# Kernel tuning notes

Hardware: AMD Instinct MI355X
Metric: run time of the kernel (lower is better)

## Reference

```python
import jax, jax.numpy as jnp
import numpy as np

B, D, T, K = 32, 64, 4096, 512
COMMITMENT_COST = 0.25


def setup_inputs() -> dict:
    key = jax.random.key(0)
    k1, k2 = jax.random.split(key)
    z = jax.random.normal(k1, (B, D, T), dtype=jnp.float32)
    # nn.Embedding init: uniform(-1/K, 1/K)
    codebook = jax.random.uniform(k2, (K, D), dtype=jnp.float32,
                                  minval=-1.0 / K, maxval=1.0 / K)
    return {"z": z, "codebook": codebook}


def reference(z, codebook):
    sg = jax.lax.stop_gradient
    zt = jnp.transpose(z, (0, 2, 1))            # [B, T, D]
    zf = zt.reshape(-1, D)                      # [N, D], N = B*T
    # squared L2 distances: ||z||^2 + ||e||^2 - 2 z.e  -> [N, K]
    dists = (jnp.sum(zf * zf, axis=1, keepdims=True)
             + jnp.sum(codebook * codebook, axis=1)
             - 2.0 * jnp.matmul(zf, codebook.T))
    idx = jnp.argmin(dists, axis=1)             # [N]
    # gather codebook rows (same math as one-hot @ codebook)
    quantized = codebook[idx].reshape(zt.shape)  # [B, T, D]
    codebook_loss = jnp.mean((sg(quantized) - zt) ** 2)
    commitment_loss = jnp.mean((quantized - sg(zt)) ** 2)
    vq_loss = codebook_loss + COMMITMENT_COST * commitment_loss
    # straight-through estimator
    quantized_st = zt + sg(quantized - zt)
    quantized_out = jnp.transpose(quantized_st, (0, 2, 1))  # [B, D, T]
    indices = idx.reshape(B, T)
    return vq_loss, quantized_out, indices
```

## Files before the change

### kernel.cpp

```cpp
#include <hip/hip_runtime.h>

#define NB 32
#define ND 64
#define NT 4096
#define NK 512
#define NGRID 1024

typedef __attribute__((ext_vector_type(8))) short short8;
typedef __attribute__((ext_vector_type(16))) float f32x16;
typedef unsigned int uint32;
typedef unsigned short ushort16_t;

#define PERM(r) ((((r) & 7) * 16) + ((r) >> 3))
#define STR 68
#define ESTR 66
#define M2 2.5e-4f
#define RCAP 4
#define NSLOT 16

__device__ __forceinline__ ushort16_t bf16rne(float f) {
    uint32 u = __float_as_uint(f);
    return (ushort16_t)((u + 0x7FFFu + ((u >> 16) & 1u)) >> 16);
}
__device__ __forceinline__ float bf16tof(ushort16_t h) {
    return __uint_as_float(((uint32)h) << 16);
}

__global__ void prep_kernel(const float* __restrict__ cb,
                            uint4* __restrict__ cbfrag,
                            float* __restrict__ enorm,
                            double* __restrict__ loss_acc,
                            uint32* __restrict__ counter) {
    const int bi = blockIdx.x, tid = threadIdx.x;
    if (bi < 16) {
        const int t = bi * 256 + tid;
        const int c = t >> 8, rem = t & 255, s = rem >> 6, L = rem & 63;
        const int kcode = c * 32 + (L & 31);
        const int dbase = s * 16 + ((L >> 5) << 3);
        const float* src = cb + (size_t)kcode * 64 + dbase;
        const float4 pa = *(const float4*)src;
        const float4 pb = *(const float4*)(src + 4);
        const float f[8] = {pa.x, pa.y, pa.z, pa.w, pb.x, pb.y, pb.z, pb.w};
        uint32 hw[4], lw[4];
#pragma unroll
        for (int i = 0; i < 4; ++i) {
            const ushort16_t h0 = bf16rne(f[2*i]);
            const ushort16_t h1 = bf16rne(f[2*i+1]);
            const ushort16_t l0 = bf16rne(f[2*i]   - bf16tof(h0));
            const ushort16_t l1 = bf16rne(f[2*i+1] - bf16tof(h1));
            hw[i] = (uint32)h0 | ((uint32)h1 << 16);
            lw[i] = (uint32)l0 | ((uint32)l1 << 16);
        }
        cbfrag[(size_t)((c*4+s)*2 + 0)*64 + L] = make_uint4(hw[0],hw[1],hw[2],hw[3]);
        cbfrag[(size_t)((c*4+s)*2 + 1)*64 + L] = make_uint4(lw[0],lw[1],lw[2],lw[3]);
    } else {
        if (tid < NSLOT) loss_acc[tid] = 0.0;
        if (tid == 0) *counter = 0u;
        for (int k = tid; k < NK; k += 256) {
            const float* e = cb + (size_t)k * ND;
            float r[8];
#pragma unroll
            for (int j = 0; j < 8; ++j) {
                float s = __fmul_rn(e[j], e[j]);
#pragma unroll
                for (int i = 1; i < 8; ++i)
                    s = __fadd_rn(s, __fmul_rn(e[8*i+j], e[8*i+j]));
                r[j] = s;
            }
            enorm[k] = __fadd_rn(__fadd_rn(__fadd_rn(r[0],r[1]), __fadd_rn(r[2],r[3])),
                                 __fadd_rn(__fadd_rn(r[4],r[5]), __fadd_rn(r[6],r[7])));
        }
    }
}

__device__ __forceinline__ float exact_dist(const float* __restrict__ zrow,
                                            const float* __restrict__ cb,
                                            const float* __restrict__ enl,
                                            float zn, int k2) {
    const float4* e4 = (const float4*)(cb + (size_t)k2 * ND);
    float a = 0.0f;
#pragma unroll
    for (int w = 0; w < 16; ++w) {
        const float4 ev = e4[w];
        const float4 zv = *(const float4*)(zrow + 4 * w);
        a = __builtin_fmaf(zv.x, ev.x, a);
        a = __builtin_fmaf(zv.y, ev.y, a);
        a = __builtin_fmaf(zv.z, ev.z, a);
        a = __builtin_fmaf(zv.w, ev.w, a);
    }
    return __fsub_rn(__fadd_rn(zn, enl[k2]), __fmul_rn(2.0f, a));
}

__global__ __launch_bounds__(256, 3) void vq_main(const float* __restrict__ z,
                                                  const float* __restrict__ cb,
                                                  const uint4* __restrict__ cbfrag,
                                                  const float* __restrict__ enorm,
                                                  float* __restrict__ qout,
                                                  float* __restrict__ idxout,
                                                  double* __restrict__ loss_acc,
                                                  uint32* __restrict__ counter,
                                                  float* __restrict__ out0) {
    __shared__ __align__(16) char smem[39968];
    float*       zl   = (float*)smem;
    float*       enl  = (float*)(smem + 34816);
    float*       znl  = (float*)(smem + 36864);
    ushort16_t*  cand = (ushort16_t*)(smem + 37376);
    int*         sfin = (int*)(smem + 39424);
    double*      sred = (double*)(smem + 39936);

    const int bi    = blockIdx.x;
    const int b     = bi >> 5;
    const int tbase = (bi & 31) * 128;
    const int tid   = threadIdx.x;
    const size_t zoff = (size_t)b * (ND * NT) + tbase;

#pragma unroll
    for (int j = 0; j < 8; ++j) {
        const int qq = j * 256 + tid;
        const int i4 = qq & 31, d = qq >> 5;
        const float4 v = *(const float4*)(z + zoff + (size_t)d * NT + i4 * 4);
        const float vv[4] = {v.x, v.y, v.z, v.w};
#pragma unroll
        for (int c = 0; c < 4; ++c) {
            const int r = i4 * 4 + c;
            zl[PERM(r) * STR + d] = vv[c];
        }
    }
    for (int k = tid; k < NK; k += 256) enl[k] = enorm[k];
    __syncthreads();

    if (tid < 128) {
        const int r = tid;
        const float4* zr4 = (const float4*)&zl[PERM(r) * STR];
        float x[64];
#pragma unroll
        for (int wq = 0; wq < 16; ++wq) {
            const float4 t4 = zr4[wq];
            x[4*wq] = t4.x; x[4*wq+1] = t4.y; x[4*wq+2] = t4.z; x[4*wq+3] = t4.w;
        }
        float r8[8];
#pragma unroll
        for (int jj = 0; jj < 8; ++jj) {
            float s = __fmul_rn(x[jj], x[jj]);
#pragma unroll
            for (int ii = 1; ii < 8; ++ii)
                s = __fadd_rn(s, __fmul_rn(x[8*ii+jj], x[8*ii+jj]));
            r8[jj] = s;
        }
        znl[r] = __fadd_rn(__fadd_rn(__fadd_rn(r8[0],r8[1]), __fadd_rn(r8[2],r8[3])),
                           __fadd_rn(__fadd_rn(r8[4],r8[5]), __fadd_rn(r8[6],r8[7])));
    }

    const int L    = tid & 63;
    const int w    = tid >> 6;
    const int h    = L >> 5;
    const int rowl = w * 32 + (L & 31);
    short8 bhf[4], blf[4];
    {
        const float* zrow = &zl[PERM(rowl) * STR];
#pragma unroll
        for (int s = 0; s < 4; ++s) {
            const int d0 = s * 16 + h * 8;
            const float4 pa = *(const float4*)(zrow + d0);
            const float4 pb = *(const float4*)(zrow + d0 + 4);
            const float f[8] = {pa.x, pa.y, pa.z, pa.w, pb.x, pb.y, pb.z, pb.w};
            uint32 hw[4], lw[4];
#pragma unroll
            for (int i = 0; i < 4; ++i) {
                const ushort16_t h0 = bf16rne(f[2*i]);
                const ushort16_t h1 = bf16rne(f[2*i+1]);
                const ushort16_t l0 = bf16rne(f[2*i]   - bf16tof(h0));
                const ushort16_t l1 = bf16rne(f[2*i+1] - bf16tof(h1));
                hw[i] = (uint32)h0 | ((uint32)h1 << 16);
                lw[i] = (uint32)l0 | ((uint32)l1 << 16);
            }
            union { uint4 u; short8 s8; } uh, ul;
            uh.u = make_uint4(hw[0],hw[1],hw[2],hw[3]);
            ul.u = make_uint4(lw[0],lw[1],lw[2],lw[3]);
            bhf[s] = uh.s8; blf[s] = ul.s8;
        }
    }
    __syncthreads();

    const int h4 = h * 4;

    uint32 p1 = 0u, p2 = 0u, p3 = 0u;
#pragma unroll 2
    for (int c = 0; c < 16; ++c) {
        uint4 B[8];
#pragma unroll
        for (int p = 0; p < 8; ++p) B[p] = cbfrag[(size_t)((c * 8 + p) * 64) + L];
        f32x16 acc0, acc1;
#pragma unroll
        for (int r = 0; r < 16; ++r) { acc0[r] = 0.0f; acc1[r] = 0.0f; }
#pragma unroll
        for (int s = 0; s < 4; ++s) {
            union { uint4 u; short8 s8; } ah, al;
            ah.u = B[s * 2 + 0];
            al.u = B[s * 2 + 1];
            acc0 = __builtin_amdgcn_mfma_f32_32x32x16_bf16(ah.s8, bhf[s], acc0, 0, 0, 0);
            acc0 = __builtin_amdgcn_mfma_f32_32x32x16_bf16(al.s8, bhf[s], acc0, 0, 0, 0);
            acc1 = __builtin_amdgcn_mfma_f32_32x32x16_bf16(ah.s8, blf[s], acc1, 0, 0, 0);
        }
#pragma unroll
        for (int r = 0; r < 16; ++r) {
            const int kc = c * 32 + ((r & 3) + 8 * (r >> 2)) + h4;
            const float a = acc0[r] + acc1[r];
            const uint32 pv = (__float_as_uint(fmaxf(a + 1.0f, 0.0f)) & ~0x1FFu)
                            | (uint32)kc;
            const bool g1 = pv > p1, g2 = pv > p2, g3 = pv > p3;
            p3 = g2 ? p2 : (g3 ? pv : p3);
            p2 = g1 ? p1 : (g2 ? pv : p2);
            p1 = g1 ? pv : p1;
        }
    }

    const uint32 op1 = __shfl_xor(p1, 32);
    const uint32 pkG = (p1 > op1) ? p1 : op1;
    const int    kG  = (int)(pkG & 0x1FFu);
    const float  bm   = __uint_as_float(pkG & ~0x1FFu) - 1.0f;
    const float  thrf = bm - M2;
    const uint32 thrF = __float_as_uint(fmaxf(thrf + 1.0f, 0.0f)) & ~0x1FFu;

    const float* zrow = &zl[PERM(rowl) * STR];
    const float  zn   = znl[rowl];
    const int    iown = (((kG >> 2) & 1) == h);

    int bkf;
    if (__any((int)(p3 >= thrF))) {
        int myc = 0, ovf = 0;
        ushort16_t* mylist = cand + (rowl * 2 + h) * RCAP;
#pragma unroll 1
        for (int c = 0; c < 16; ++c) {
            uint4 B[8];
#pragma unroll
            for (int p = 0; p < 8; ++p) B[p] = cbfrag[(size_t)((c * 8 + p) * 64) + L];
            f32x16 acc0, acc1;
#pragma unroll
            for (int r = 0; r < 16; ++r) { acc0[r] = 0.0f; acc1[r] = 0.0f; }
#pragma unroll
            for (int s = 0; s < 4; ++s) {
                union { uint4 u; short8 s8; } ah, al;
                ah.u = B[s * 2 + 0];
                al.u = B[s * 2 + 1];
                acc0 = __builtin_amdgcn_mfma_f32_32x32x16_bf16(ah.s8, bhf[s], acc0, 0, 0, 0);
                acc0 = __builtin_amdgcn_mfma_f32_32x32x16_bf16(al.s8, bhf[s], acc0, 0, 0, 0);
                acc1 = __builtin_amdgcn_mfma_f32_32x32x16_bf16(ah.s8, blf[s], acc1, 0, 0, 0);
            }
#pragma unroll
            for (int r = 0; r < 16; ++r) {
                const int kc = c * 32 + ((r & 3) + 8 * (r >> 2)) + h4;
                const float a = acc0[r] + acc1[r];
                const uint32 pv = (__float_as_uint(fmaxf(a + 1.0f, 0.0f)) & ~0x1FFu)
                                | (uint32)kc;
                if (pv >= thrF && kc != kG) {
                    if (myc < RCAP) mylist[myc++] = (ushort16_t)kc;
                    else ovf = 1;
                }
            }
        }
        const int totr = myc + __shfl_xor(myc, 32);
        const int aovf = ovf | __shfl_xor(ovf, 32);
        if (aovf) {
            float bd = __builtin_inff(); bkf = 0x7FFFFFFF;
            for (int c = 0; c < 16; ++c)
#pragma unroll
                for (int qd = 0; qd < 4; ++qd)
#pragma unroll
                    for (int i = 0; i < 4; ++i) {
                        const int k2c = c * 32 + qd * 8 + h * 4 + i;
                        const float dv = exact_dist(zrow, cb, enl, zn, k2c);
                        if (dv < bd || (dv == bd && k2c < bkf)) { bd = dv; bkf = k2c; }
                    }
            const float obd = __shfl_xor(bd, 32);
            const int   obq = __shfl_xor(bkf, 32);
            if (obd < bd || (obd == bd && obq < bkf)) bkf = obq;
        } else if (totr > 0) {
            float bd = __builtin_inff(); bkf = 0x7FFFFFFF;
            if (iown) { bd = exact_dist(zrow, cb, enl, zn, kG); bkf = kG; }
            for (int i = 0; i < myc; ++i) {
                const int k2c = mylist[i];
                const float dv = exact_dist(zrow, cb, enl, zn, k2c);
                if (dv < bd || (dv == bd && k2c < bkf)) { bd = dv; bkf = k2c; }
            }
            const float obd = __shfl_xor(bd, 32);
            const int   obq = __shfl_xor(bkf, 32);
            if (obd < bd || (obd == bd && obq < bkf)) bkf = obq;
        } else {
            bkf = kG;
        }
    } else {
        const int k1 = (int)(p1 & 0x1FFu);
        const int k2 = (int)(p2 & 0x1FFu);
        const int r1v = (!iown) && (p1 >= thrF);
        const int r2v = (p2 >= thrF);
        const int nr  = r1v + r2v;
        const int totr = nr + __shfl_xor(nr, 32);
        if (totr > 0) {
            float bd = __builtin_inff(); bkf = 0x7FFFFFFF;
            if (iown) { bd = exact_dist(zrow, cb, enl, zn, kG); bkf = kG; }
            if (r1v) {
                const float dv = exact_dist(zrow, cb, enl, zn, k1);
                if (dv < bd || (dv == bd && k1 < bkf)) { bd = dv; bkf = k1; }
            }
            if (r2v) {
                const float dv = exact_dist(zrow, cb, enl, zn, k2);
                if (dv < bd || (dv == bd && k2 < bkf)) { bd = dv; bkf = k2; }
            }
            const float obd = __shfl_xor(bd, 32);
            const int   obq = __shfl_xor(bkf, 32);
            if (obd < bd || (obd == bd && obq < bkf)) bkf = obq;
        } else {
            bkf = kG;
        }
    }

    if (h == 0) {
        sfin[rowl] = bkf;
        idxout[(size_t)b * NT + tbase + rowl] = (float)bkf;
    }
    __syncthreads();

    float* ech = zl;
#pragma unroll
    for (int j = 0; j < 8; ++j) {
        const int qq  = j * 256 + tid;
        const int row = qq >> 4, d4 = qq & 15;
        const float4 v = *(const float4*)(cb + (size_t)sfin[row] * ND + d4 * 4);
        float* dst = &ech[row * ESTR + d4 * 4];
        *(float2*)(dst)     = make_float2(v.x, v.y);
        *(float2*)(dst + 2) = make_float2(v.z, v.w);
    }
    __syncthreads();

    double lsum = 0.0;
#pragma unroll 4
    for (int j = 0; j < 8; ++j) {
        const int qq  = j * 256 + tid;
        const int ir0 = (qq & 31) * 4, d = qq >> 5;
        const float4 zv4 = *(const float4*)(z + zoff + (size_t)d * NT + ir0);
        const float zv[4] = {zv4.x, zv4.y, zv4.z, zv4.w};
        float qo[4];
#pragma unroll
        for (int m = 0; m < 4; ++m) {
            const float ev = ech[(ir0 + m) * ESTR + d];
            const float diff = __fsub_rn(ev, zv[m]);
            qo[m] = __fadd_rn(zv[m], diff);
            lsum += (double)diff * (double)diff;
        }
        *(float4*)(qout + (size_t)b * (ND*NT) + (size_t)d * NT + tbase + ir0) =
            make_float4(qo[0], qo[1], qo[2], qo[3]);
    }
#pragma unroll
    for (int off = 32; off > 0; off >>= 1) lsum += __shfl_down(lsum, off, 64);
    if ((tid & 63) == 0) sred[tid >> 6] = lsum;
    __syncthreads();

    if (tid == 0) {
        const double bsum = (sred[0] + sred[1]) + (sred[2] + sred[3]);
        atomicAdd(loss_acc + (bi & (NSLOT - 1)), bsum);
        __threadfence();
        const uint32 old = atomicAdd(counter, 1u);
        if (old == (uint32)(NGRID - 1)) {
            __threadfence();
            double tot = 0.0;
            for (int i = 0; i < NSLOT; ++i)
                tot += ((volatile double*)loss_acc)[i];
            const double m = tot / (double)((size_t)NB * NT * ND);
            out0[0] = (float)(1.25 * m);
        }
    }
}

extern "C" void kernel_launch(void* const* d_in, const int* in_sizes, int n_in,
                              void* d_out, int out_size, void* d_ws, size_t ws_size,
                              hipStream_t stream) {
    const float* z  = (const float*)d_in[0];
    const float* cb = (const float*)d_in[1];

    float* out      = (float*)d_out;
    float* loss_out = out;
    float* qout     = out + 1;
    float* idxout   = out + 1 + (size_t)NB * ND * NT;

    uint4*  cbfrag   = (uint4*)d_ws;
    float*  enorm    = (float*)((char*)d_ws + 139264);
    double* loss_acc = (double*)((char*)d_ws + 141312);
    uint32* counter  = (uint32*)((char*)d_ws + 141440);

    prep_kernel<<<17, 256, 0, stream>>>(cb, cbfrag, enorm, loss_acc, counter);
    vq_main<<<NGRID, 256, 0, stream>>>(z, cb, cbfrag, enorm, qout, idxout,
                                       loss_acc, counter, loss_out);
}
```

Before: 178.9 us.

## Process two row tiles per wave to reuse codebook fragments across MFMAs

Halves the block to 128 threads (two waves) and makes each wave handle 64 rows instead of 32, so every codebook fragment loaded from global memory feeds MFMAs for two row tiles. Each A fragment load is amortized over twice the MFMA work, and the interleaved independent accumulators give more instruction-level parallelism. The cost is roughly doubled register pressure (two accumulator sets, two sets of B fragments, two top-3 trackers) and fewer waves per block, which may reduce occupancy and latency hiding.

```diff
diff --git a/kernel.cpp b/kernel.cpp
--- a/kernel.cpp
+++ b/kernel.cpp
@@ -91,7 +91,7 @@
     return __fsub_rn(__fadd_rn(zn, enl[k2]), __fmul_rn(2.0f, a));
 }
 
-__global__ __launch_bounds__(256, 3) void vq_main(const float* __restrict__ z,
+__global__ __launch_bounds__(128, 2) void vq_main(const float* __restrict__ z,
                                                   const float* __restrict__ cb,
                                                   const uint4* __restrict__ cbfrag,
                                                   const float* __restrict__ enorm,
@@ -115,8 +115,8 @@
     const size_t zoff = (size_t)b * (ND * NT) + tbase;
 
 #pragma unroll
-    for (int j = 0; j < 8; ++j) {
-        const int qq = j * 256 + tid;
+    for (int j = 0; j < 16; ++j) {
+        const int qq = j * 128 + tid;
         const int i4 = qq & 31, d = qq >> 5;
         const float4 v = *(const float4*)(z + zoff + (size_t)d * NT + i4 * 4);
         const float vv[4] = {v.x, v.y, v.z, v.w};
@@ -126,10 +126,10 @@
             zl[PERM(r) * STR + d] = vv[c];
         }
     }
-    for (int k = tid; k < NK; k += 256) enl[k] = enorm[k];
+    for (int k = tid; k < NK; k += 128) enl[k] = enorm[k];
     __syncthreads();
 
-    if (tid < 128) {
+    {
         const int r = tid;
         const float4* zr4 = (const float4*)&zl[PERM(r) * STR];
         float x[64];
@@ -154,10 +154,14 @@
     const int L    = tid & 63;
     const int w    = tid >> 6;
     const int h    = L >> 5;
-    const int rowl = w * 32 + (L & 31);
-    short8 bhf[4], blf[4];
-    {
-        const float* zrow = &zl[PERM(rowl) * STR];
+    const int rowl0 = w * 64 + (L & 31);
+    const int rowl1 = rowl0 + 32;
+    short8 bhf0[4], blf0[4], bhf1[4], blf1[4];
+    __syncthreads();
+#pragma unroll
+    for (int t = 0; t < 2; ++t) {
+        const int rl = (t == 0) ? rowl0 : rowl1;
+        const float* zrow = &zl[PERM(rl) * STR];
 #pragma unroll
         for (int s = 0; s < 4; ++s) {
             const int d0 = s * 16 + h * 8;
@@ -177,154 +181,186 @@
             union { uint4 u; short8 s8; } uh, ul;
             uh.u = make_uint4(hw[0],hw[1],hw[2],hw[3]);
             ul.u = make_uint4(lw[0],lw[1],lw[2],lw[3]);
-            bhf[s] = uh.s8; blf[s] = ul.s8;
-        }
-    }
-    __syncthreads();
+            if (t == 0) { bhf0[s] = uh.s8; blf0[s] = ul.s8; }
+            else        { bhf1[s] = uh.s8; blf1[s] = ul.s8; }
+        }
+    }
 
     const int h4 = h * 4;
 
-    uint32 p1 = 0u, p2 = 0u, p3 = 0u;
+    uint32 P1[2] = {0u, 0u}, P2[2] = {0u, 0u}, P3[2] = {0u, 0u};
 #pragma unroll 2
     for (int c = 0; c < 16; ++c) {
         uint4 B[8];
 #pragma unroll
         for (int p = 0; p < 8; ++p) B[p] = cbfrag[(size_t)((c * 8 + p) * 64) + L];
-        f32x16 acc0, acc1;
-#pragma unroll
-        for (int r = 0; r < 16; ++r) { acc0[r] = 0.0f; acc1[r] = 0.0f; }
+        f32x16 A0, A1;
+#pragma unroll
+        for (int r = 0; r < 16; ++r) { A0[r] = 0.0f; A1[r] = 0.0f; }
 #pragma unroll
         for (int s = 0; s < 4; ++s) {
             union { uint4 u; short8 s8; } ah, al;
             ah.u = B[s * 2 + 0];
             al.u = B[s * 2 + 1];
-            acc0 = __builtin_amdgcn_mfma_f32_32x32x16_bf16(ah.s8, bhf[s], acc0, 0, 0, 0);
-            acc0 = __builtin_amdgcn_mfma_f32_32x32x16_bf16(al.s8, bhf[s], acc0, 0, 0, 0);
-            acc1 = __builtin_amdgcn_mfma_f32_32x32x16_bf16(ah.s8, blf[s], acc1, 0, 0, 0);
+            A0 = __builtin_amdgcn_mfma_f32_32x32x16_bf16(ah.s8, bhf0[s], A0, 0, 0, 0);
+            A1 = __builtin_amdgcn_mfma_f32_32x32x16_bf16(ah.s8, bhf1[s], A1, 0, 0, 0);
+            A0 = __builtin_amdgcn_mfma_f32_32x32x16_bf16(al.s8, bhf0[s], A0, 0, 0, 0);
+            A1 = __builtin_amdgcn_mfma_f32_32x32x16_bf16(al.s8, bhf1[s], A1, 0, 0, 0);
+            A0 = __builtin_amdgcn_mfma_f32_32x32x16_bf16(ah.s8, blf0[s], A0, 0, 0, 0);
+            A1 = __builtin_amdgcn_mfma_f32_32x32x16_bf16(ah.s8, blf1[s], A1, 0, 0, 0);
         }
 #pragma unroll
         for (int r = 0; r < 16; ++r) {
             const int kc = c * 32 + ((r & 3) + 8 * (r >> 2)) + h4;
-            const float a = acc0[r] + acc1[r];
-            const uint32 pv = (__float_as_uint(fmaxf(a + 1.0f, 0.0f)) & ~0x1FFu)
-                            | (uint32)kc;
-            const bool g1 = pv > p1, g2 = pv > p2, g3 = pv > p3;
-            p3 = g2 ? p2 : (g3 ? pv : p3);
-            p2 = g1 ? p1 : (g2 ? pv : p2);
-            p1 = g1 ? pv : p1;
-        }
-    }
-
-    const uint32 op1 = __shfl_xor(p1, 32);
-    const uint32 pkG = (p1 > op1) ? p1 : op1;
-    const int    kG  = (int)(pkG & 0x1FFu);
-    const float  bm   = __uint_as_float(pkG & ~0x1FFu) - 1.0f;
-    const float  thrf = bm - M2;
-    const uint32 thrF = __float_as_uint(fmaxf(thrf + 1.0f, 0.0f)) & ~0x1FFu;
-
-    const float* zrow = &zl[PERM(rowl) * STR];
-    const float  zn   = znl[rowl];
-    const int    iown = (((kG >> 2) & 1) == h);
-
-    int bkf;
-    if (__any((int)(p3 >= thrF))) {
-        int myc = 0, ovf = 0;
-        ushort16_t* mylist = cand + (rowl * 2 + h) * RCAP;
+            {
+                const uint32 pv = (__float_as_uint(fmaxf(A0[r] + 1.0f, 0.0f)) & ~0x1FFu)
+                                | (uint32)kc;
+                const bool g1 = pv > P1[0], g2 = pv > P2[0], g3 = pv > P3[0];
+                P3[0] = g2 ? P2[0] : (g3 ? pv : P3[0]);
+                P2[0] = g1 ? P1[0] : (g2 ? pv : P2[0]);
+                P1[0] = g1 ? pv : P1[0];
+            }
+            {
+                const uint32 pv = (__float_as_uint(fmaxf(A1[r] + 1.0f, 0.0f)) & ~0x1FFu)
+                                | (uint32)kc;
+                const bool g1 = pv > P1[1], g2 = pv > P2[1], g3 = pv > P3[1];
+                P3[1] = g2 ? P2[1] : (g3 ? pv : P3[1]);
+                P2[1] = g1 ? P1[1] : (g2 ? pv : P2[1]);
+                P1[1] = g1 ? pv : P1[1];
+            }
+        }
+    }
+
+    int    kG[2], iown[2];
+    uint32 thrF[2];
+#pragma unroll
+    for (int t = 0; t < 2; ++t) {
+        const uint32 op1 = __shfl_xor(P1[t], 32);
+        const uint32 pk  = (P1[t] > op1) ? P1[t] : op1;
+        kG[t] = (int)(pk & 0x1FFu);
+        const float bm   = __uint_as_float(pk & ~0x1FFu) - 1.0f;
+        const float thrf = bm - M2;
+        thrF[t] = __float_as_uint(fmaxf(thrf + 1.0f, 0.0f)) & ~0x1FFu;
+        iown[t] = (((kG[t] >> 2) & 1) == h);
+    }
+
+    const float* zrowR[2] = { &zl[PERM(rowl0) * STR], &zl[PERM(rowl1) * STR] };
+    const float  znR[2]   = { znl[rowl0], znl[rowl1] };
+
+    int bkf[2];
+    if (__any((int)(P3[0] >= thrF[0]) | (int)(P3[1] >= thrF[1]))) {
+        int myc[2] = {0, 0}, ovf = 0;
+        ushort16_t* ml[2] = { cand + (rowl0 * 2 + h) * RCAP,
+                              cand + (rowl1 * 2 + h) * RCAP };
 #pragma unroll 1
         for (int c = 0; c < 16; ++c) {
             uint4 B[8];
 #pragma unroll
             for (int p = 0; p < 8; ++p) B[p] = cbfrag[(size_t)((c * 8 + p) * 64) + L];
-            f32x16 acc0, acc1;
-#pragma unroll
-            for (int r = 0; r < 16; ++r) { acc0[r] = 0.0f; acc1[r] = 0.0f; }
+            f32x16 A0, A1;
+#pragma unroll
+            for (int r = 0; r < 16; ++r) { A0[r] = 0.0f; A1[r] = 0.0f; }
 #pragma unroll
             for (int s = 0; s < 4; ++s) {
                 union { uint4 u; short8 s8; } ah, al;
                 ah.u = B[s * 2 + 0];
                 al.u = B[s * 2 + 1];
-                acc0 = __builtin_amdgcn_mfma_f32_32x32x16_bf16(ah.s8, bhf[s], acc0, 0, 0, 0);
-                acc0 = __builtin_amdgcn_mfma_f32_32x32x16_bf16(al.s8, bhf[s], acc0, 0, 0, 0);
-                acc1 = __builtin_amdgcn_mfma_f32_32x32x16_bf16(ah.s8, blf[s], acc1, 0, 0, 0);
+                A0 = __builtin_amdgcn_mfma_f32_32x32x16_bf16(ah.s8, bhf0[s], A0, 0, 0, 0);
+                A1 = __builtin_amdgcn_mfma_f32_32x32x16_bf16(ah.s8, bhf1[s], A1, 0, 0, 0);
+                A0 = __builtin_amdgcn_mfma_f32_32x32x16_bf16(al.s8, bhf0[s], A0, 0, 0, 0);
+                A1 = __builtin_amdgcn_mfma_f32_32x32x16_bf16(al.s8, bhf1[s], A1, 0, 0, 0);
+                A0 = __builtin_amdgcn_mfma_f32_32x32x16_bf16(ah.s8, blf0[s], A0, 0, 0, 0);
+                A1 = __builtin_amdgcn_mfma_f32_32x32x16_bf16(ah.s8, blf1[s], A1, 0, 0, 0);
             }
 #pragma unroll
             for (int r = 0; r < 16; ++r) {
                 const int kc = c * 32 + ((r & 3) + 8 * (r >> 2)) + h4;
-                const float a = acc0[r] + acc1[r];
-                const uint32 pv = (__float_as_uint(fmaxf(a + 1.0f, 0.0f)) & ~0x1FFu)
-                                | (uint32)kc;
-                if (pv >= thrF && kc != kG) {
-                    if (myc < RCAP) mylist[myc++] = (ushort16_t)kc;
-                    else ovf = 1;
+#pragma unroll
+                for (int t = 0; t < 2; ++t) {
+                    const float av = (t == 0) ? A0[r] : A1[r];
+                    const uint32 pv = (__float_as_uint(fmaxf(av + 1.0f, 0.0f)) & ~0x1FFu)
+                                    | (uint32)kc;
+                    if (pv >= thrF[t] && kc != kG[t]) {
+                        if (myc[t] < RCAP) ml[t][myc[t]++] = (ushort16_t)kc;
+                        else ovf = 1;
+                    }
                 }
             }
         }
-        const int totr = myc + __shfl_xor(myc, 32);
         const int aovf = ovf | __shfl_xor(ovf, 32);
-        if (aovf) {
-            float bd = __builtin_inff(); bkf = 0x7FFFFFFF;
-            for (int c = 0; c < 16; ++c)
-#pragma unroll
-                for (int qd = 0; qd < 4; ++qd)
-#pragma unroll
-                    for (int i = 0; i < 4; ++i) {
-                        const int k2c = c * 32 + qd * 8 + h * 4 + i;
-                        const float dv = exact_dist(zrow, cb, enl, zn, k2c);
-                        if (dv < bd || (dv == bd && k2c < bkf)) { bd = dv; bkf = k2c; }
-                    }
-            const float obd = __shfl_xor(bd, 32);
-            const int   obq = __shfl_xor(bkf, 32);
-            if (obd < bd || (obd == bd && obq < bkf)) bkf = obq;
-        } else if (totr > 0) {
-            float bd = __builtin_inff(); bkf = 0x7FFFFFFF;
-            if (iown) { bd = exact_dist(zrow, cb, enl, zn, kG); bkf = kG; }
-            for (int i = 0; i < myc; ++i) {
-                const int k2c = mylist[i];
-                const float dv = exact_dist(zrow, cb, enl, zn, k2c);
-                if (dv < bd || (dv == bd && k2c < bkf)) { bd = dv; bkf = k2c; }
-            }
-            const float obd = __shfl_xor(bd, 32);
-            const int   obq = __shfl_xor(bkf, 32);
-            if (obd < bd || (obd == bd && obq < bkf)) bkf = obq;
-        } else {
-            bkf = kG;
+#pragma unroll
+        for (int t = 0; t < 2; ++t) {
+            const int totr = myc[t] + __shfl_xor(myc[t], 32);
+            if (aovf) {
+                float bd = __builtin_inff(); int bq = 0x7FFFFFFF;
+                for (int c = 0; c < 16; ++c)
+#pragma unroll
+                    for (int qd = 0; qd < 4; ++qd)
+#pragma unroll
+                        for (int i = 0; i < 4; ++i) {
+                            const int k2c = c * 32 + qd * 8 + h * 4 + i;
+                            const float dv = exact_dist(zrowR[t], cb, enl, znR[t], k2c);
+                            if (dv < bd || (dv == bd && k2c < bq)) { bd = dv; bq = k2c; }
+                        }
+                const float obd = __shfl_xor(bd, 32);
+                const int   obq = __shfl_xor(bq, 32);
+                bkf[t] = (obd < bd || (obd == bd && obq < bq)) ? obq : bq;
+            } else if (totr > 0) {
+                float bd = __builtin_inff(); int bq = 0x7FFFFFFF;
+                if (iown[t]) { bd = exact_dist(zrowR[t], cb, enl, znR[t], kG[t]); bq = kG[t]; }
+                for (int i = 0; i < myc[t]; ++i) {
+                    const int k2c = ml[t][i];
+                    const float dv = exact_dist(zrowR[t], cb, enl, znR[t], k2c);
+                    if (dv < bd || (dv == bd && k2c < bq)) { bd = dv; bq = k2c; }
+                }
+                const float obd = __shfl_xor(bd, 32);
+                const int   obq = __shfl_xor(bq, 32);
+                bkf[t] = (obd < bd || (obd == bd && obq < bq)) ? obq : bq;
+            } else {
+                bkf[t] = kG[t];
+            }
         }
     } else {
-        const int k1 = (int)(p1 & 0x1FFu);
-        const int k2 = (int)(p2 & 0x1FFu);
-        const int r1v = (!iown) && (p1 >= thrF);
-        const int r2v = (p2 >= thrF);
-        const int nr  = r1v + r2v;
-        const int totr = nr + __shfl_xor(nr, 32);
-        if (totr > 0) {
-            float bd = __builtin_inff(); bkf = 0x7FFFFFFF;
-            if (iown) { bd = exact_dist(zrow, cb, enl, zn, kG); bkf = kG; }
-            if (r1v) {
-                const float dv = exact_dist(zrow, cb, enl, zn, k1);
-                if (dv < bd || (dv == bd && k1 < bkf)) { bd = dv; bkf = k1; }
-            }
-            if (r2v) {
-                const float dv = exact_dist(zrow, cb, enl, zn, k2);
-                if (dv < bd || (dv == bd && k2 < bkf)) { bd = dv; bkf = k2; }
-            }
-            const float obd = __shfl_xor(bd, 32);
-            const int   obq = __shfl_xor(bkf, 32);
-            if (obd < bd || (obd == bd && obq < bkf)) bkf = obq;
-        } else {
-            bkf = kG;
+#pragma unroll
+        for (int t = 0; t < 2; ++t) {
+            const int k1 = (int)(P1[t] & 0x1FFu);
+            const int k2 = (int)(P2[t] & 0x1FFu);
+            const int r1v = (!iown[t]) && (P1[t] >= thrF[t]);
+            const int r2v = (P2[t] >= thrF[t]);
+            const int nr  = r1v + r2v;
+            const int totr = nr + __shfl_xor(nr, 32);
+            if (totr > 0) {
+                float bd = __builtin_inff(); int bq = 0x7FFFFFFF;
+                if (iown[t]) { bd = exact_dist(zrowR[t], cb, enl, znR[t], kG[t]); bq = kG[t]; }
+                if (r1v) {
+                    const float dv = exact_dist(zrowR[t], cb, enl, znR[t], k1);
+                    if (dv < bd || (dv == bd && k1 < bq)) { bd = dv; bq = k1; }
+                }
+                if (r2v) {
+                    const float dv = exact_dist(zrowR[t], cb, enl, znR[t], k2);
+                    if (dv < bd || (dv == bd && k2 < bq)) { bd = dv; bq = k2; }
+                }
+                const float obd = __shfl_xor(bd, 32);
+                const int   obq = __shfl_xor(bq, 32);
+                bkf[t] = (obd < bd || (obd == bd && obq < bq)) ? obq : bq;
+            } else {
+                bkf[t] = kG[t];
+            }
         }
     }
 
     if (h == 0) {
-        sfin[rowl] = bkf;
-        idxout[(size_t)b * NT + tbase + rowl] = (float)bkf;
+        sfin[rowl0] = bkf[0];
+        sfin[rowl1] = bkf[1];
+        idxout[(size_t)b * NT + tbase + rowl0] = (float)bkf[0];
+        idxout[(size_t)b * NT + tbase + rowl1] = (float)bkf[1];
     }
     __syncthreads();
 
     float* ech = zl;
 #pragma unroll
-    for (int j = 0; j < 8; ++j) {
-        const int qq  = j * 256 + tid;
+    for (int j = 0; j < 16; ++j) {
+        const int qq  = j * 128 + tid;
         const int row = qq >> 4, d4 = qq & 15;
         const float4 v = *(const float4*)(cb + (size_t)sfin[row] * ND + d4 * 4);
         float* dst = &ech[row * ESTR + d4 * 4];
@@ -335,8 +371,8 @@
 
     double lsum = 0.0;
 #pragma unroll 4
-    for (int j = 0; j < 8; ++j) {
-        const int qq  = j * 256 + tid;
+    for (int j = 0; j < 16; ++j) {
+        const int qq  = j * 128 + tid;
         const int ir0 = (qq & 31) * 4, d = qq >> 5;
         const float4 zv4 = *(const float4*)(z + zoff + (size_t)d * NT + ir0);
         const float zv[4] = {zv4.x, zv4.y, zv4.z, zv4.w};
@@ -357,7 +393,7 @@
     __syncthreads();
 
     if (tid == 0) {
-        const double bsum = (sred[0] + sred[1]) + (sred[2] + sred[3]);
+        const double bsum = sred[0] + sred[1];
         atomicAdd(loss_acc + (bi & (NSLOT - 1)), bsum);
         __threadfence();
         const uint32 old = atomicAdd(counter, 1u);
@@ -389,6 +425,6 @@
     uint32* counter  = (uint32*)((char*)d_ws + 141440);
 
     prep_kernel<<<17, 256, 0, stream>>>(cb, cbfrag, enorm, loss_acc, counter);
-    vq_main<<<NGRID, 256, 0, stream>>>(z, cb, cbfrag, enorm, qout, idxout,
+    vq_main<<<NGRID, 128, 0, stream>>>(z, cb, cbfrag, enorm, qout, idxout,
                                        loss_acc, counter, loss_out);
 }
```

Result: slower. 186.8 us (+4.4%).
